# Kernel tuning notes

Hardware: AMD Instinct MI355X
Metric: run time of the kernel (lower is better)

The kernel has to match this reference:

```python
import jax, jax.numpy as jnp
import numpy as np

B, T, C, HS = 8, 4096, 1024, 128
BLOCK = 4096  # block_size; T == BLOCK here


def _pyr_mask(bs):
    # Faithful numpy translation of the torch 'pyr' buffer construction.
    h = bs // 2
    top = np.repeat(np.flip(np.tril(np.ones((h, h), np.float32)), axis=1), 2, axis=0)  # (bs, h)
    reps = np.array([2] * (h - 1) + [1])
    bot = np.concatenate(
        [np.zeros((1, h), np.float32),
         np.repeat(np.tril(np.ones((h, h), np.float32)), reps, axis=0)], axis=0)  # (bs, h)
    return np.concatenate([top, bot], axis=1)  # (bs, bs)


def setup_inputs() -> dict:
    key = jax.random.key(0)
    kx, kq, kk, kv = jax.random.split(key, 4)
    s = C ** -0.5
    x = jax.random.normal(kx, (B, T, C), jnp.float32)
    Wq = jax.random.normal(kq, (C, HS), jnp.float32) * s
    Wk = jax.random.normal(kk, (C, HS), jnp.float32) * s
    Wv = jax.random.normal(kv, (C, HS), jnp.float32) * s
    return {"x": x, "Wq": Wq, "Wk": Wk, "Wv": Wv}


def reference(x, Wq, Wk, Wv):
    Tlen = x.shape[1]
    start = (BLOCK - Tlen) // 2
    end = BLOCK + (-(BLOCK - Tlen)) // 2  # python floor-div, matches torch slicing
    mask = jnp.asarray(_pyr_mask(BLOCK)[:Tlen, start:end])  # (T, T) 0/1

    q = x @ Wq  # (B, T, HS)
    k = x @ Wk
    v = x @ Wv
    wei = jnp.einsum('btd,bsd->bts', q, k) * (HS ** -0.5)  # (B, T, T)
    wei = jnp.where(mask == 0, -jnp.inf, wei)  # bidirectional_mode == 'bi'
    wei = jax.nn.softmax(wei, axis=-1)
    # dropout p=0.0 -> identity
    return wei @ v  # (B, T, HS)
```

## Files before the change

kernel.cpp:

```cpp
#include <hip/hip_runtime.h>

typedef unsigned short u16;
typedef __attribute__((ext_vector_type(8))) short bf16x8;
typedef __attribute__((ext_vector_type(8))) unsigned short u16x8;
typedef __attribute__((ext_vector_type(4))) float f32x4;
typedef __attribute__((ext_vector_type(4))) unsigned short u16x4;
typedef __attribute__((ext_vector_type(2))) unsigned int u32x2;
typedef __attribute__((ext_vector_type(4))) unsigned int u32x4;

#define Bn 8
#define Tn 4096
#define Cn 1024
#define HSn 128

#define SBAR __builtin_amdgcn_sched_barrier(0)

__device__ __forceinline__ float bf2f(u16 b) {
    unsigned u = ((unsigned)b) << 16;
    return __builtin_bit_cast(float, u);
}
__device__ __forceinline__ unsigned cvt_pk_bf16(float a, float b) {
    unsigned r;
    asm("v_cvt_pk_bf16_f32 %0, %1, %2" : "=v"(r) : "v"(a), "v"(b));
    return r;
}
__device__ __forceinline__ u16 f2bf(float f) { return (u16)cvt_pk_bf16(f, f); }

__device__ __forceinline__ void wg_barrier() {
    __builtin_amdgcn_sched_barrier(0);
    asm volatile("s_waitcnt lgkmcnt(0)" ::: "memory");
    __builtin_amdgcn_s_barrier();
    __builtin_amdgcn_sched_barrier(0);
}

__device__ __forceinline__ void dma16(const void* g, void* l) {
    __builtin_amdgcn_global_load_lds(
        (const __attribute__((address_space(1))) unsigned int*)g,
        (__attribute__((address_space(3))) unsigned int*)l, 16, 0, 0);
}

extern "C" __global__ __launch_bounds__(256) void head_wtrans(
    const float* __restrict__ Wq, const float* __restrict__ Wk,
    const float* __restrict__ Wv, u16* __restrict__ wt) {
    const float* W = (blockIdx.y == 0) ? Wq : (blockIdx.y == 1) ? Wk : Wv;
    const float scale =
        (blockIdx.y == 0) ? (0.08838834764831845f * 1.4426950408889634f) : 1.0f;
    u16* o = wt + (size_t)blockIdx.y * Cn * HSn;
    int tid = blockIdx.x * 256 + threadIdx.x;
    int n = tid >> 10, kk = tid & 1023;
    o[tid] = f2bf(W[kk * HSn + n] * scale);
}

extern "C" __global__ __launch_bounds__(512) void head_proj(
    const float* __restrict__ x, const u16* __restrict__ wt, u16* __restrict__ qo,
    u16* __restrict__ ko, u16* __restrict__ vto) {
    __shared__ __align__(16) unsigned char sh[3 * 40960];
    const int tid = threadIdx.x;
    const int w = tid >> 6, l = tid & 63, quad = l >> 4, ln = l & 15;
    const int bm0 = blockIdx.x * 128;
    const int mg = w & 1, ng = w >> 1;
    const int m0 = mg * 64, n0 = ng * 96;

    const f32x4 zero4 = {0.f, 0.f, 0.f, 0.f};
    f32x4 acc[4][6];
#pragma unroll
    for (int fi = 0; fi < 4; fi++)
#pragma unroll
        for (int ci = 0; ci < 6; ci++) acc[fi][ci] = zero4;

    const float* xg[2];
    int xd[2];
#pragma unroll
    for (int p = 0; p < 2; p++) {
        int s = p * 512 + tid;
        int row = s >> 3, slot = s & 7;
        int g = slot ^ (row & 7);
        xg[p] = x + (size_t)(bm0 + row) * Cn + g * 4;
        xd[p] = s * 16;
    }
    const u16* wg[3];
    int wd[3];
#pragma unroll
    for (int p = 0; p < 3; p++) {
        int s = p * 512 + tid;
        int row = s >> 2, slot = s & 3;
        int g = slot ^ ((row >> 1) & 3);
        wg[p] = wt + (size_t)(row >> 7) * (Cn * HSn) + (size_t)(row & 127) * Cn + g * 8;
        wd[p] = 16384 + s * 16;
    }

    int aoff[4];
#pragma unroll
    for (int fi = 0; fi < 4; fi++) {
        int row = m0 + fi * 16 + ln;
        aoff[fi] = row * 128 + (((2 * quad) ^ (row & 7)) * 16);
    }
    int boff[6];
#pragma unroll
    for (int ci = 0; ci < 6; ci++) {
        int c = n0 + ci * 16 + ln;
        boff[ci] = 16384 + c * 64 + ((quad ^ ((c >> 1) & 3)) * 16);
    }

#define P_ISSUE(BUF, KT)                                      \
    do {                                                      \
        dma16(xg[0] + (KT) * 32, sh + (BUF) * 40960 + xd[0]); \
        dma16(xg[1] + (KT) * 32, sh + (BUF) * 40960 + xd[1]); \
        dma16(wg[0] + (KT) * 32, sh + (BUF) * 40960 + wd[0]); \
        dma16(wg[1] + (KT) * 32, sh + (BUF) * 40960 + wd[1]); \
        dma16(wg[2] + (KT) * 32, sh + (BUF) * 40960 + wd[2]); \
    } while (0)

#define P_COMPUTE(BUF)                                                     \
    do {                                                                   \
        const unsigned char* cbase = sh + (BUF) * 40960;                   \
        bf16x8 af[4];                                                      \
        _Pragma("unroll") for (int fi = 0; fi < 4; fi++) {                 \
            f32x4 lo = *(const f32x4*)(cbase + aoff[fi]);                  \
            f32x4 hi = *(const f32x4*)(cbase + (aoff[fi] ^ 16));           \
            u32x4 tt;                                                      \
            tt[0] = cvt_pk_bf16(lo[0], lo[1]);                             \
            tt[1] = cvt_pk_bf16(lo[2], lo[3]);                             \
            tt[2] = cvt_pk_bf16(hi[0], hi[1]);                             \
            tt[3] = cvt_pk_bf16(hi[2], hi[3]);                             \
            af[fi] = __builtin_bit_cast(bf16x8, tt);                       \
        }                                                                  \
        _Pragma("unroll") for (int ci = 0; ci < 6; ci++) {                 \
            bf16x8 bfr = *(const bf16x8*)(cbase + boff[ci]);               \
            _Pragma("unroll") for (int fi = 0; fi < 4; fi++)               \
                acc[fi][ci] = __builtin_amdgcn_mfma_f32_16x16x32_bf16(     \
                    af[fi], bfr, acc[fi][ci], 0, 0, 0);                    \
        }                                                                  \
    } while (0)

    P_ISSUE(0, 0);
    P_ISSUE(1, 1);
    P_ISSUE(2, 2);
    SBAR;
    asm volatile("s_waitcnt vmcnt(10)" ::: "memory");
    __builtin_amdgcn_s_barrier();
    SBAR;

    int cur = 0;
    for (int t = 0; t < 32; ++t) {
        P_COMPUTE(cur);
        wg_barrier();
        if (t + 3 < 32) P_ISSUE(cur, t + 3);
        SBAR;
        if (t <= 28)
            asm volatile("s_waitcnt vmcnt(10)" ::: "memory");
        else if (t == 29)
            asm volatile("s_waitcnt vmcnt(5)" ::: "memory");
        else if (t == 30)
            asm volatile("s_waitcnt vmcnt(0)" ::: "memory");
        __builtin_amdgcn_s_barrier();
        SBAR;
        cur = (cur == 2) ? 0 : cur + 1;
    }
#undef P_ISSUE
#undef P_COMPUTE

    u16* const tL = (u16*)sh;
#pragma unroll
    for (int ci = 0; ci < 6; ci++) {
        int col = n0 + ci * 16 + ln;
        int cin = col & 127;
        int sidx = col >> 7;
#pragma unroll
        for (int fi = 0; fi < 4; fi++) {
            int grow = bm0 + m0 + fi * 16 + quad * 4;
            if (sidx == 0) {
#pragma unroll
                for (int r = 0; r < 4; r++)
                    qo[(size_t)(grow + r) * HSn + cin] = f2bf(acc[fi][ci][r]);
            } else if (sidx == 1) {
#pragma unroll
                for (int r = 0; r < 4; r++)
                    ko[(size_t)(grow + r) * HSn + cin] = f2bf(acc[fi][ci][r]);
            } else {
                u16x4 pk4;
#pragma unroll
                for (int r = 0; r < 4; r++) pk4[r] = f2bf(acc[fi][ci][r]);
                *(u16x4*)(tL + cin * 136 + (m0 + fi * 16 + quad * 4)) = pk4;
            }
        }
    }
    wg_barrier();
    {
        const int bb = bm0 >> 12, t0b = bm0 & 4095;
        const int dl = tid >> 4, tch = (tid & 15) * 8;
#pragma unroll
        for (int dp = 0; dp < 4; dp++) {
            int d = dp * 32 + dl;
            u16x8 vv = *(const u16x8*)(tL + d * 136 + tch);
            *(u16x8*)(vto + ((size_t)bb * HSn + d) * Tn + t0b + tch) = vv;
        }
    }
}

extern "C" __global__ __launch_bounds__(512) void head_flash_chunk(
    const u16* __restrict__ q, const u16* __restrict__ k, const u16* __restrict__ vt,
    u16* __restrict__ Opart, float* __restrict__ lsum) {
    __shared__ __align__(16) u16 kL[64 * 136];
    __shared__ __align__(16) u16 vL[128 * 72];
    __shared__ __align__(16) u16 pL[8 * 16 * 72];
    const int tid = threadIdx.x;
    const int w = tid >> 6, l = tid & 63, quad = l >> 4, ln = l & 15;
    const int cid = blockIdx.x;
    const int grp = cid >> 4;
    const int qbi = (grp < 16) ? (31 - grp) : (grp - 16);
    const int b = (cid >> 1) & 7;
    const int half = cid & 1;
    const int q0 = qbi * 128;
    const int qrow = q0 + w * 16;

    const int rkBase = tid >> 4, ckK = tid & 15;
    const int rvBase = tid >> 3, ckV = tid & 7;

    bf16x8 qf[4];
#pragma unroll
    for (int ks = 0; ks < 4; ks++)
        qf[ks] = *(const bf16x8*)(q + ((size_t)b * Tn + qrow + ln) * HSn + ks * 32 +
                                  quad * 8);

    const f32x4 zero4 = {0.f, 0.f, 0.f, 0.f};
    float l2 = 0.f;
    const int qme = qrow + ln;
    const int clo = 2047 - (qme >> 1), chi = 2047 + ((qme + 1) >> 1);
    const int cloW0 = 2047 - (qrow >> 1);
    const int chiW0 = 2047 + ((qrow + 1) >> 1);
    const int cloMin = 2047 - ((qrow + 15) >> 1);
    const int chiMax = 2047 + ((qrow + 16) >> 1);
    f32x4 o[8];
#pragma unroll
    for (int dt = 0; dt < 8; dt++) o[dt] = zero4;

    const int qmax = q0 + 127;
    const int tlo = (2047 - (qmax >> 1)) >> 6;
    const int thi = (2047 + ((qmax + 1) >> 1)) >> 6;
    const int W = thi - tlo + 1;
    const int c0 = (W + 1) >> 1;
    const int kstart = half ? tlo + c0 : tlo;
    const int kend = half ? thi : tlo + c0 - 1;

    u16x8 pk[2], pv[2];
    {
        const int t0 = kstart * 64;
#pragma unroll
        for (int p = 0; p < 2; p++)
            pk[p] = *(const u16x8*)(k + ((size_t)b * Tn + t0 + p * 32 + rkBase) * HSn +
                                    ckK * 8);
#pragma unroll
        for (int p = 0; p < 2; p++)
            pv[p] = *(const u16x8*)(vt + ((size_t)b * HSn + p * 64 + rvBase) * Tn + t0 +
                                    ckV * 8);
    }

    for (int kt = kstart; kt <= kend; kt++) {
        const int t0 = kt * 64;
        wg_barrier();
#pragma unroll
        for (int p = 0; p < 2; p++)
            *(u16x8*)(kL + (p * 32 + rkBase) * 136 + ckK * 8) = pk[p];
#pragma unroll
        for (int p = 0; p < 2; p++)
            *(u16x8*)(vL + (p * 64 + rvBase) * 72 + ckV * 8) = pv[p];
        if (kt < kend) {
            const int t1 = t0 + 64;
#pragma unroll
            for (int p = 0; p < 2; p++)
                pk[p] = *(const u16x8*)(k + ((size_t)b * Tn + t1 + p * 32 + rkBase) * HSn +
                                        ckK * 8);
#pragma unroll
            for (int p = 0; p < 2; p++)
                pv[p] = *(const u16x8*)(vt + ((size_t)b * HSn + p * 64 + rvBase) * Tn +
                                        t1 + ckV * 8);
        }
        wg_barrier();

        const bool live = !((t0 + 63 < cloMin) || (t0 > chiMax));

        if (live) {
            f32x4 s[4];
#pragma unroll
            for (int nt = 0; nt < 4; nt++) s[nt] = zero4;
            __builtin_amdgcn_s_setprio(1);
#pragma unroll
            for (int nt = 0; nt < 4; nt++) {
                int R = nt * 16 + ln;
#pragma unroll
                for (int ks = 0; ks < 4; ks++) {
                    bf16x8 kf = *(const bf16x8*)(kL + R * 136 + (ks * 4 + quad) * 8);
                    s[nt] =
                        __builtin_amdgcn_mfma_f32_16x16x32_bf16(kf, qf[ks], s[nt], 0, 0, 0);
                }
            }
            __builtin_amdgcn_s_setprio(0);
            if (t0 < cloW0 || t0 + 63 > chiW0) {
#pragma unroll
                for (int nt = 0; nt < 4; nt++)
#pragma unroll
                    for (int r = 0; r < 4; r++) {
                        int t = t0 + nt * 16 + quad * 4 + r;
                        bool valid = (t >= clo) && (t <= chi);
                        s[nt][r] = valid ? s[nt][r] : -1e30f;
                    }
            }
            float ls = 0.f;
#pragma unroll
            for (int nt = 0; nt < 4; nt++) {
                float p0 = exp2f(s[nt][0]), p1 = exp2f(s[nt][1]);
                float p2 = exp2f(s[nt][2]), p3 = exp2f(s[nt][3]);
                ls += (p0 + p1) + (p2 + p3);
                u32x2 d;
                d.x = cvt_pk_bf16(p0, p1);
                d.y = cvt_pk_bf16(p2, p3);
                *(u32x2*)(pL + w * 1152 + ln * 72 + nt * 16 + quad * 4) = d;
            }
            l2 += ls;
            __builtin_amdgcn_s_setprio(1);
#pragma unroll
            for (int jt = 0; jt < 2; jt++) {
                bf16x8 pf = *(const bf16x8*)(pL + w * 1152 + ln * 72 + jt * 32 + quad * 8);
#pragma unroll
                for (int dt = 0; dt < 8; dt++) {
                    int R = dt * 16 + ln;
                    bf16x8 vf = *(const bf16x8*)(vL + R * 72 + (jt * 4 + quad) * 8);
                    o[dt] = __builtin_amdgcn_mfma_f32_16x16x32_bf16(pf, vf, o[dt], 0, 0, 0);
                }
            }
            __builtin_amdgcn_s_setprio(0);
        }
    }
    l2 += __shfl_xor(l2, 16, 64);
    l2 += __shfl_xor(l2, 32, 64);
#pragma unroll
    for (int dt = 0; dt < 8; dt++)
#pragma unroll
        for (int r = 0; r < 4; r++)
            Opart[((size_t)cid * 128 + w * 16 + quad * 4 + r) * HSn + dt * 16 + ln] =
                f2bf(o[dt][r]);
    if (l < 16) lsum[(size_t)cid * 128 + w * 16 + ln] = l2;
}

extern "C" __global__ __launch_bounds__(256) void head_combine(
    const u16* __restrict__ Opart, const float* __restrict__ lsum,
    float* __restrict__ out) {
    const int bid = blockIdx.x;
    const int qb64 = bid >> 3, b = bid & 7;
    const int tid = threadIdx.x;
    const int row = tid >> 2, dseg = (tid & 3) * 32;
    const int qbi = qb64 >> 1;
    const int inrow = (qb64 & 1) * 64 + row;
    const int grp0 = (qbi >= 16) ? (31 - qbi) : (qbi + 16);
    const int cid0 = grp0 * 16 + b * 2;
    const size_t r0 = (size_t)cid0 * 128 + inrow, r1 = r0 + 128;
    float l0 = lsum[r0], l1 = lsum[r1];
    float inv = 1.0f / (l0 + l1);
    float* op = out + ((size_t)b * Tn + qb64 * 64 + row) * HSn + dseg;
    const u16* p0 = Opart + r0 * HSn + dseg;
    const u16* p1 = Opart + r1 * HSn + dseg;
#pragma unroll
    for (int j = 0; j < 4; j++) {
        u16x8 a = *(const u16x8*)(p0 + j * 8);
        u16x8 c = *(const u16x8*)(p1 + j * 8);
        f32x4 o1, o2;
#pragma unroll
        for (int e = 0; e < 4; e++) o1[e] = (bf2f(a[e]) + bf2f(c[e])) * inv;
#pragma unroll
        for (int e = 0; e < 4; e++) o2[e] = (bf2f(a[4 + e]) + bf2f(c[4 + e])) * inv;
        *(f32x4*)(op + j * 8) = o1;
        *(f32x4*)(op + j * 8 + 4) = o2;
    }
}

extern "C" __global__ __launch_bounds__(256) void head_flash(
    const u16* __restrict__ q, const u16* __restrict__ k, const u16* __restrict__ vt,
    float* __restrict__ out) {
    __shared__ __align__(16) u16 kL[64 * 136];
    __shared__ __align__(16) u16 vL[128 * 72];
    __shared__ __align__(16) u16 pL[4 * 16 * 72];
    const int tid = threadIdx.x;
    const int w = tid >> 6, l = tid & 63, quad = l >> 4, ln = l & 15;
    const int bx = blockIdx.x;
    const int half = bx >> 8, idx = bx & 255;
    const int p5 = idx & 31, b = idx >> 5;
    const int qb = half ? p5 : 63 - p5;
    const int q0 = qb * 64;
    const int qrow = q0 + w * 16;
    const int rkBase = tid >> 4, ckK = tid & 15;
    const int rvBase = tid >> 3, ckV = tid & 7;

    bf16x8 qf[4];
#pragma unroll
    for (int ks = 0; ks < 4; ks++)
        qf[ks] = *(const bf16x8*)(q + ((size_t)b * Tn + qrow + ln) * HSn + ks * 32 +
                                  quad * 8);
    const f32x4 zero4 = {0.f, 0.f, 0.f, 0.f};
    float m2 = -1e30f, l2 = 0.f;
    const int qme = qrow + ln;
    const int clo = 2047 - (qme >> 1), chi = 2047 + ((qme + 1) >> 1);
    f32x4 o[8];
#pragma unroll
    for (int dt = 0; dt < 8; dt++) o[dt] = zero4;
    const int qmax = q0 + 63;
    const int tlo = (2047 - (qmax >> 1)) >> 6;
    const int thi = (2047 + ((qmax + 1) >> 1)) >> 6;

    u16x8 pk[4], pv[4];
    {
        const int t0 = tlo * 64;
#pragma unroll
        for (int p = 0; p < 4; p++)
            pk[p] = *(const u16x8*)(k + ((size_t)b * Tn + t0 + p * 16 + rkBase) * HSn +
                                    ckK * 8);
#pragma unroll
        for (int p = 0; p < 4; p++)
            pv[p] = *(const u16x8*)(vt + ((size_t)b * HSn + p * 32 + rvBase) * Tn + t0 +
                                    ckV * 8);
    }
    for (int kt = tlo; kt <= thi; kt++) {
        const int t0 = kt * 64;
        __syncthreads();
#pragma unroll
        for (int p = 0; p < 4; p++)
            *(u16x8*)(kL + (p * 16 + rkBase) * 136 + ckK * 8) = pk[p];
#pragma unroll
        for (int p = 0; p < 4; p++)
            *(u16x8*)(vL + (p * 32 + rvBase) * 72 + ckV * 8) = pv[p];
        if (kt < thi) {
            const int t1 = t0 + 64;
#pragma unroll
            for (int p = 0; p < 4; p++)
                pk[p] = *(const u16x8*)(k + ((size_t)b * Tn + t1 + p * 16 + rkBase) * HSn +
                                        ckK * 8);
#pragma unroll
            for (int p = 0; p < 4; p++)
                pv[p] = *(const u16x8*)(vt + ((size_t)b * HSn + p * 32 + rvBase) * Tn +
                                        t1 + ckV * 8);
        }
        __syncthreads();
        f32x4 s[4];
#pragma unroll
        for (int nt = 0; nt < 4; nt++) s[nt] = zero4;
#pragma unroll
        for (int nt = 0; nt < 4; nt++) {
            int R = nt * 16 + ln;
#pragma unroll
            for (int ks = 0; ks < 4; ks++) {
                bf16x8 kf = *(const bf16x8*)(kL + R * 136 + (ks * 4 + quad) * 8);
                s[nt] = __builtin_amdgcn_mfma_f32_16x16x32_bf16(kf, qf[ks], s[nt], 0, 0, 0);
            }
        }
#pragma unroll
        for (int nt = 0; nt < 4; nt++)
#pragma unroll
            for (int r = 0; r < 4; r++) {
                int t = t0 + nt * 16 + quad * 4 + r;
                bool valid = (t >= clo) && (t <= chi);
                s[nt][r] = valid ? s[nt][r] : -1e30f;
            }
        float mc = s[0][0];
#pragma unroll
        for (int nt = 0; nt < 4; nt++)
#pragma unroll
            for (int r = 0; r < 4; r++) mc = fmaxf(mc, s[nt][r]);
        mc = fmaxf(mc, __shfl_xor(mc, 16, 64));
        mc = fmaxf(mc, __shfl_xor(mc, 32, 64));
        float mn = fmaxf(m2, mc);
        float alpha = exp2f(m2 - mn);
        m2 = mn;
        float ls = 0.f;
#pragma unroll
        for (int nt = 0; nt < 4; nt++) {
            float p0 = exp2f(s[nt][0] - mn), p1 = exp2f(s[nt][1] - mn);
            float p2 = exp2f(s[nt][2] - mn), p3 = exp2f(s[nt][3] - mn);
            ls += (p0 + p1) + (p2 + p3);
            u32x2 d;
            d.x = cvt_pk_bf16(p0, p1);
            d.y = cvt_pk_bf16(p2, p3);
            *(u32x2*)(pL + w * 1152 + ln * 72 + nt * 16 + quad * 4) = d;
        }
        ls += __shfl_xor(ls, 16, 64);
        ls += __shfl_xor(ls, 32, 64);
        l2 = l2 * alpha + ls;
        float aR[4];
#pragma unroll
        for (int r = 0; r < 4; r++) aR[r] = __shfl(alpha, quad * 4 + r, 64);
#pragma unroll
        for (int dt = 0; dt < 8; dt++) {
            f32x4 oo = o[dt];
#pragma unroll
            for (int r = 0; r < 4; r++) oo[r] *= aR[r];
            o[dt] = oo;
        }
#pragma unroll
        for (int jt = 0; jt < 2; jt++) {
            bf16x8 pf = *(const bf16x8*)(pL + w * 1152 + ln * 72 + jt * 32 + quad * 8);
#pragma unroll
            for (int dt = 0; dt < 8; dt++) {
                int R = dt * 16 + ln;
                bf16x8 vf = *(const bf16x8*)(vL + R * 72 + (jt * 4 + quad) * 8);
                o[dt] = __builtin_amdgcn_mfma_f32_16x16x32_bf16(pf, vf, o[dt], 0, 0, 0);
            }
        }
    }
    float inv = 1.0f / l2;
    float rl[4];
#pragma unroll
    for (int r = 0; r < 4; r++) rl[r] = __shfl(inv, quad * 4 + r, 64);
#pragma unroll
    for (int dt = 0; dt < 8; dt++)
#pragma unroll
        for (int r = 0; r < 4; r++) {
            int row = qrow + quad * 4 + r;
            out[((size_t)b * Tn + row) * HSn + dt * 16 + ln] = o[dt][r] * rl[r];
        }
}

extern "C" void kernel_launch(void* const* d_in, const int* in_sizes, int n_in,
                              void* d_out, int out_size, void* d_ws, size_t ws_size,
                              hipStream_t stream) {
    const float* x = (const float*)d_in[0];
    const float* Wq = (const float*)d_in[1];
    const float* Wk = (const float*)d_in[2];
    const float* Wv = (const float*)d_in[3];
    float* outp = (float*)d_out;
    char* ws = (char*)d_ws;
    u16* wt = (u16*)(ws);
    u16* qb = (u16*)(ws + (1u << 20));
    u16* kb = (u16*)(ws + (9u << 20));
    u16* vtb = (u16*)(ws + (17u << 20));
    u16* Opart = (u16*)(ws + (25u << 20));
    float* lsum = (float*)(ws + (42u << 20));

    head_wtrans<<<dim3(512, 3), 256, 0, stream>>>(Wq, Wk, Wv, wt);
    head_proj<<<dim3(256), 512, 0, stream>>>(x, wt, qb, kb, vtb);
    if (ws_size >= (44ull << 20)) {
        head_flash_chunk<<<dim3(512), 512, 0, stream>>>(qb, kb, vtb, Opart, lsum);
        head_combine<<<dim3(512), 256, 0, stream>>>(Opart, lsum, outp);
    } else {
        head_flash<<<dim3(512), 256, 0, stream>>>(qb, kb, vtb, outp);
    }
}
```

Measured before the change: 297.0 us.

## Shrink projection tiles and load weight fragments directly into registers

The QKV projection kernel now uses 64-row tiles with 256 threads and 512 blocks instead of 128-row tiles with 512 threads. Only x is staged through LDS via DMA, while each wave loads its B fragments straight from global memory into three rotating register buffers two steps ahead. This removes the weight tiles from LDS, cutting shared memory from about 120KB to 24KB so more blocks fit per CU. In exchange, each weight element is re-read from global/L2 by twice as many blocks, and register pressure goes up.

```diff
diff --git a/kernel.cpp b/kernel.cpp
--- a/kernel.cpp
+++ b/kernel.cpp
@@ -51,15 +51,14 @@
     o[tid] = f2bf(W[kk * HSn + n] * scale);
 }
 
-extern "C" __global__ __launch_bounds__(512) void head_proj(
+extern "C" __global__ __launch_bounds__(256) void head_proj(
     const float* __restrict__ x, const u16* __restrict__ wt, u16* __restrict__ qo,
     u16* __restrict__ ko, u16* __restrict__ vto) {
-    __shared__ __align__(16) unsigned char sh[3 * 40960];
+    __shared__ __align__(16) unsigned char sh[3 * 8192];
     const int tid = threadIdx.x;
     const int w = tid >> 6, l = tid & 63, quad = l >> 4, ln = l & 15;
-    const int bm0 = blockIdx.x * 128;
-    const int mg = w & 1, ng = w >> 1;
-    const int m0 = mg * 64, n0 = ng * 96;
+    const int bm0 = blockIdx.x * 64;
+    const int n0 = w * 96;
 
     const f32x4 zero4 = {0.f, 0.f, 0.f, 0.f};
     f32x4 acc[4][6];
@@ -72,52 +71,42 @@
     int xd[2];
 #pragma unroll
     for (int p = 0; p < 2; p++) {
-        int s = p * 512 + tid;
+        int s = p * 256 + tid;
         int row = s >> 3, slot = s & 7;
         int g = slot ^ (row & 7);
         xg[p] = x + (size_t)(bm0 + row) * Cn + g * 4;
         xd[p] = s * 16;
     }
-    const u16* wg[3];
-    int wd[3];
-#pragma unroll
-    for (int p = 0; p < 3; p++) {
-        int s = p * 512 + tid;
-        int row = s >> 2, slot = s & 3;
-        int g = slot ^ ((row >> 1) & 3);
-        wg[p] = wt + (size_t)(row >> 7) * (Cn * HSn) + (size_t)(row & 127) * Cn + g * 8;
-        wd[p] = 16384 + s * 16;
-    }
-
     int aoff[4];
 #pragma unroll
     for (int fi = 0; fi < 4; fi++) {
-        int row = m0 + fi * 16 + ln;
+        int row = fi * 16 + ln;
         aoff[fi] = row * 128 + (((2 * quad) ^ (row & 7)) * 16);
     }
-    int boff[6];
-#pragma unroll
-    for (int ci = 0; ci < 6; ci++) {
-        int c = n0 + ci * 16 + ln;
-        boff[ci] = 16384 + c * 64 + ((quad ^ ((c >> 1) & 3)) * 16);
-    }
-
-#define P_ISSUE(BUF, KT)                                      \
-    do {                                                      \
-        dma16(xg[0] + (KT) * 32, sh + (BUF) * 40960 + xd[0]); \
-        dma16(xg[1] + (KT) * 32, sh + (BUF) * 40960 + xd[1]); \
-        dma16(wg[0] + (KT) * 32, sh + (BUF) * 40960 + wd[0]); \
-        dma16(wg[1] + (KT) * 32, sh + (BUF) * 40960 + wd[1]); \
-        dma16(wg[2] + (KT) * 32, sh + (BUF) * 40960 + wd[2]); \
+    const u16* bp[6];
+#pragma unroll
+    for (int ci = 0; ci < 6; ci++)
+        bp[ci] = wt + (size_t)(n0 + ci * 16 + ln) * Cn + quad * 8;
+
+#define P_DMA(BUF, KT)                                       \
+    do {                                                     \
+        dma16(xg[0] + (KT) * 32, sh + (BUF) * 8192 + xd[0]); \
+        dma16(xg[1] + (KT) * 32, sh + (BUF) * 8192 + xd[1]); \
     } while (0)
 
-#define P_COMPUTE(BUF)                                                     \
+#define P_LOADB(DST, KT)                                   \
+    do {                                                   \
+        _Pragma("unroll") for (int ci = 0; ci < 6; ci++)   \
+            DST[ci] = *(const u16x8*)(bp[ci] + (KT) * 32); \
+    } while (0)
+
+#define P_COMPUTE(BUF, BREG)                                               \
     do {                                                                   \
-        const unsigned char* cbase = sh + (BUF) * 40960;                   \
+        const unsigned char* cb = sh + (BUF) * 8192;                       \
         bf16x8 af[4];                                                      \
         _Pragma("unroll") for (int fi = 0; fi < 4; fi++) {                 \
-            f32x4 lo = *(const f32x4*)(cbase + aoff[fi]);                  \
-            f32x4 hi = *(const f32x4*)(cbase + (aoff[fi] ^ 16));           \
+            f32x4 lo = *(const f32x4*)(cb + aoff[fi]);                     \
+            f32x4 hi = *(const f32x4*)(cb + (aoff[fi] ^ 16));              \
             u32x4 tt;                                                      \
             tt[0] = cvt_pk_bf16(lo[0], lo[1]);                             \
             tt[1] = cvt_pk_bf16(lo[2], lo[3]);                             \
@@ -126,39 +115,53 @@
             af[fi] = __builtin_bit_cast(bf16x8, tt);                       \
         }                                                                  \
         _Pragma("unroll") for (int ci = 0; ci < 6; ci++) {                 \
-            bf16x8 bfr = *(const bf16x8*)(cbase + boff[ci]);               \
+            bf16x8 bfr = __builtin_bit_cast(bf16x8, BREG[ci]);             \
             _Pragma("unroll") for (int fi = 0; fi < 4; fi++)               \
                 acc[fi][ci] = __builtin_amdgcn_mfma_f32_16x16x32_bf16(     \
                     af[fi], bfr, acc[fi][ci], 0, 0, 0);                    \
         }                                                                  \
     } while (0)
 
-    P_ISSUE(0, 0);
-    P_ISSUE(1, 1);
-    P_ISSUE(2, 2);
+#define P_PHASE(T, BUF, BCUR, BNXT)                                         \
+    do {                                                                    \
+        int t_ = (T);                                                       \
+        if (t_ < 32) {                                                      \
+            P_COMPUTE(BUF, BCUR);                                           \
+            wg_barrier();                                                   \
+            if (t_ + 2 < 32) P_LOADB(BNXT, t_ + 2);                         \
+            if (t_ + 3 < 32) P_DMA(BUF, t_ + 3);                            \
+            SBAR;                                                           \
+            if (t_ <= 28)                                                   \
+                asm volatile("s_waitcnt vmcnt(16)" ::: "memory");           \
+            else if (t_ == 29)                                              \
+                asm volatile("s_waitcnt vmcnt(14)" ::: "memory");           \
+            else if (t_ == 30)                                              \
+                asm volatile("s_waitcnt vmcnt(6)" ::: "memory");            \
+            if (t_ < 31) __builtin_amdgcn_s_barrier();                      \
+            SBAR;                                                           \
+        }                                                                   \
+    } while (0)
+
+    u16x8 b0[6], b1[6], b2[6];
+    P_DMA(0, 0);
+    P_LOADB(b0, 0);
+    P_DMA(1, 1);
+    P_LOADB(b1, 1);
+    P_DMA(2, 2);
     SBAR;
-    asm volatile("s_waitcnt vmcnt(10)" ::: "memory");
+    asm volatile("s_waitcnt vmcnt(16)" ::: "memory");
     __builtin_amdgcn_s_barrier();
     SBAR;
 
-    int cur = 0;
-    for (int t = 0; t < 32; ++t) {
-        P_COMPUTE(cur);
-        wg_barrier();
-        if (t + 3 < 32) P_ISSUE(cur, t + 3);
-        SBAR;
-        if (t <= 28)
-            asm volatile("s_waitcnt vmcnt(10)" ::: "memory");
-        else if (t == 29)
-            asm volatile("s_waitcnt vmcnt(5)" ::: "memory");
-        else if (t == 30)
-            asm volatile("s_waitcnt vmcnt(0)" ::: "memory");
-        __builtin_amdgcn_s_barrier();
-        SBAR;
-        cur = (cur == 2) ? 0 : cur + 1;
-    }
-#undef P_ISSUE
+    for (int t3 = 0; t3 < 33; t3 += 3) {
+        P_PHASE(t3 + 0, 0, b0, b2);
+        P_PHASE(t3 + 1, 1, b1, b0);
+        P_PHASE(t3 + 2, 2, b2, b1);
+    }
+#undef P_DMA
+#undef P_LOADB
 #undef P_COMPUTE
+#undef P_PHASE
 
     u16* const tL = (u16*)sh;
 #pragma unroll
@@ -168,7 +171,7 @@
         int sidx = col >> 7;
 #pragma unroll
         for (int fi = 0; fi < 4; fi++) {
-            int grow = bm0 + m0 + fi * 16 + quad * 4;
+            int grow = bm0 + fi * 16 + quad * 4;
             if (sidx == 0) {
 #pragma unroll
                 for (int r = 0; r < 4; r++)
@@ -181,18 +184,18 @@
                 u16x4 pk4;
 #pragma unroll
                 for (int r = 0; r < 4; r++) pk4[r] = f2bf(acc[fi][ci][r]);
-                *(u16x4*)(tL + cin * 136 + (m0 + fi * 16 + quad * 4)) = pk4;
+                *(u16x4*)(tL + cin * 80 + (fi * 16 + quad * 4)) = pk4;
             }
         }
     }
     wg_barrier();
     {
         const int bb = bm0 >> 12, t0b = bm0 & 4095;
-        const int dl = tid >> 4, tch = (tid & 15) * 8;
+        const int dl = tid >> 3, tch = (tid & 7) * 8;
 #pragma unroll
         for (int dp = 0; dp < 4; dp++) {
             int d = dp * 32 + dl;
-            u16x8 vv = *(const u16x8*)(tL + d * 136 + tch);
+            u16x8 vv = *(const u16x8*)(tL + d * 80 + tch);
             *(u16x8*)(vto + ((size_t)bb * HSn + d) * Tn + t0b + tch) = vv;
         }
     }
@@ -535,7 +538,7 @@
     float* lsum = (float*)(ws + (42u << 20));
 
     head_wtrans<<<dim3(512, 3), 256, 0, stream>>>(Wq, Wk, Wv, wt);
-    head_proj<<<dim3(256), 512, 0, stream>>>(x, wt, qb, kb, vtb);
+    head_proj<<<dim3(512), 256, 0, stream>>>(x, wt, qb, kb, vtb);
     if (ws_size >= (44ull << 20)) {
         head_flash_chunk<<<dim3(512), 512, 0, stream>>>(qb, kb, vtb, Opart, lsum);
         head_combine<<<dim3(512), 256, 0, stream>>>(Opart, lsum, outp);
```

After: 310.5 us. 1.05x slower.
